# Kernel optimization log

Measured on AMD Instinct MI355X. Metric: run time of the kernel, lower is better.

## Reference

```python
import jax, jax.numpy as jnp
import numpy as np

B, N, M, C = 256, 2048, 64, 512
OUT = 3 * M + 6  # fc_write output: [M,1,1,3,1,M,M]


def setup_inputs() -> dict:
    key = jax.random.key(0)
    k0, k1, k2, k3, k4 = jax.random.split(key, 5)
    xavier = 1.4 * np.sqrt(6.0 / (C + OUT))  # xavier_uniform gain=1.4 scale
    return {
        "h": jax.random.normal(k0, (B, C), jnp.float32),
        "w_prev": jax.nn.softmax(jax.random.normal(k1, (B, N), jnp.float32), axis=1),
        "memory": jax.random.normal(k2, (B, N, M), jnp.float32),
        "W": jax.random.uniform(k3, (OUT, C), jnp.float32, -xavier, xavier),
        "b": 0.01 * jax.random.normal(k4, (OUT,), jnp.float32),
    }


def reference(h, w_prev, memory, W, b):
    # controller projection + split
    o = h @ W.T + b  # [B, 3M+6]
    bounds = np.cumsum([M, 1, 1, 3, 1, M])
    k, beta, g, s, gamma, e, a = jnp.split(o, bounds, axis=1)
    beta = jax.nn.softplus(beta)            # [B,1]
    g = jax.nn.sigmoid(g)                   # [B,1]
    s = jax.nn.softmax(s, axis=1)           # [B,3] shift weights {-1,0,+1}
    gamma = 1.0 + jax.nn.softplus(gamma)    # [B,1]
    e = jax.nn.sigmoid(e)                   # [B,M]

    # content addressing: cosine similarity + softmax
    mem_e = memory + 1e-16
    k_e = k + 1e-16
    sim = jnp.einsum('bnm,bm->bn', mem_e, k_e)
    denom = jnp.maximum(
        jnp.linalg.norm(mem_e, axis=-1) * jnp.linalg.norm(k_e, axis=-1, keepdims=True),
        1e-8,
    )
    w_c = jax.nn.softmax(beta * sim / denom, axis=1)  # [B,N]

    # interpolation gate
    w_g = g * w_c + (1.0 - g) * w_prev

    # circular shift convolution (3 taps)
    w_t = (jnp.roll(w_g, 1, axis=1) * s[:, 0:1]
           + w_g * s[:, 1:2]
           + jnp.roll(w_g, -1, axis=1) * s[:, 2:3])

    # sharpening
    w_s = w_t ** gamma
    w = w_s / (jnp.sum(w_s, axis=1, keepdims=True) + 1e-16)  # [B,N]

    # erase/add memory write
    erase = jnp.einsum('bn,bm->bnm', w, e)
    add = jnp.einsum('bn,bm->bnm', w, a)
    mem_new = memory * (1.0 - erase) + add
    return w, mem_new
```

## Files before the change

### kernel.cpp

```cpp
#include <hip/hip_runtime.h>
#include <stdint.h>

#define BB   256
#define NN   2048
#define MM   64
#define CC   512
#define OUTD 198

typedef float vf4 __attribute__((ext_vector_type(4)));

__device__ __forceinline__ float softplusf(float x) {
    return x > 20.f ? x : log1pf(expf(x));
}
__device__ __forceinline__ float sigmoidf(float x) {
    return 1.f / (1.f + expf(-x));
}

__global__ __launch_bounds__(1024, 4) void k_fused(
        const float* __restrict__ h, const float* __restrict__ Wm,
        const float* __restrict__ bias, const float* __restrict__ w_prev,
        const float* __restrict__ mem, float* __restrict__ w_out,
        float* __restrict__ mem_out) {
    __shared__ float hs[CC];
    __shared__ float os[OUTD];
    __shared__ __align__(16) float kk[MM];
    __shared__ __align__(16) float ee[MM];
    __shared__ __align__(16) float aa[MM];
    __shared__ float sc[8];
    __shared__ float lg[NN];
    __shared__ float wg[NN];
    __shared__ float red[16];

    const int b = blockIdx.x;
    const int t = threadIdx.x;
    const int lane = t & 63;
    const int wid = t >> 6;

    if (t < CC) hs[t] = h[(size_t)b * CC + t];
    __syncthreads();

    if (t < 4 * OUTD) {
        const int row = t >> 2, l4 = t & 3;
        const float* wr = Wm + (size_t)row * CC + 4 * l4;
        float acc = 0.f;
        #pragma unroll
        for (int c = 0; c < CC; c += 16) {
            const float4 p = *(const float4*)(wr + c);
            const int hb = c + 4 * l4;
            acc += p.x * hs[hb] + p.y * hs[hb + 1] + p.z * hs[hb + 2] + p.w * hs[hb + 3];
        }
        acc += __shfl_xor(acc, 1, 64);
        acc += __shfl_xor(acc, 2, 64);
        if (l4 == 0) os[row] = acc + bias[row];
    }
    __syncthreads();

    if (t < 64) {
        const float kv = os[t] + 1e-16f;
        kk[t] = kv;
        float ss = kv * kv;
        #pragma unroll
        for (int off = 32; off; off >>= 1) ss += __shfl_xor(ss, off, 64);
        if (t == 0) sc[3] = sqrtf(ss);
    } else if (t < 128) {
        const int m = t - 64;
        ee[m] = sigmoidf(os[70 + m]);
        aa[m] = os[134 + m];
    } else if (t == 128) {
        sc[0] = softplusf(os[64]);
    } else if (t == 129) {
        sc[1] = sigmoidf(os[65]);
    } else if (t == 130) {
        sc[2] = 1.f + softplusf(os[69]);
    } else if (t == 131) {
        const float x0 = os[66], x1 = os[67], x2 = os[68];
        const float mx = fmaxf(x0, fmaxf(x1, x2));
        const float e0 = expf(x0 - mx), e1 = expf(x1 - mx), e2 = expf(x2 - mx);
        const float inv = 1.f / (e0 + e1 + e2);
        sc[4] = e0 * inv; sc[5] = e1 * inv; sc[6] = e2 * inv;
    }
    __syncthreads();

    {
        const int l = t & 15, grp = t >> 4;
        const float kv0 = kk[4 * l + 0], kv1 = kk[4 * l + 1];
        const float kv2 = kk[4 * l + 2], kv3 = kk[4 * l + 3];
        const float beta = sc[0], knorm = sc[3];
        const float* mb = mem + (size_t)b * NN * MM;
        #pragma unroll 4
        for (int it = 0; it < 32; ++it) {
            const int row = it * 64 + grp;
            const float4 p = *(const float4*)(mb + (size_t)row * MM + 4 * l);
            const float m0 = p.x + 1e-16f, m1 = p.y + 1e-16f;
            const float m2 = p.z + 1e-16f, m3 = p.w + 1e-16f;
            float dot = m0 * kv0 + m1 * kv1 + m2 * kv2 + m3 * kv3;
            float ss  = m0 * m0 + m1 * m1 + m2 * m2 + m3 * m3;
            #pragma unroll
            for (int off = 1; off < 16; off <<= 1) {
                dot += __shfl_xor(dot, off, 64);
                ss  += __shfl_xor(ss,  off, 64);
            }
            if (l == 0)
                lg[row] = beta * dot / fmaxf(sqrtf(ss) * knorm, 1e-8f);
        }
    }
    __syncthreads();

    const float g = sc[1], gamma = sc[2];
    const float s0 = sc[4], s1 = sc[5], s2 = sc[6];

    float v0 = lg[t], v1 = lg[t + 1024];
    float lmax = fmaxf(v0, v1);
    #pragma unroll
    for (int off = 32; off; off >>= 1) lmax = fmaxf(lmax, __shfl_xor(lmax, off, 64));
    if (lane == 0) red[wid] = lmax;
    __syncthreads();
    float mx = red[0];
    #pragma unroll
    for (int i = 1; i < 16; ++i) mx = fmaxf(mx, red[i]);
    __syncthreads();

    v0 = expf(v0 - mx); v1 = expf(v1 - mx);
    float lsum = v0 + v1;
    #pragma unroll
    for (int off = 32; off; off >>= 1) lsum += __shfl_xor(lsum, off, 64);
    if (lane == 0) red[wid] = lsum;
    __syncthreads();
    float tot = 0.f;
    #pragma unroll
    for (int i = 0; i < 16; ++i) tot += red[i];
    __syncthreads();
    const float inv = 1.f / tot;

    wg[t]        = g * (v0 * inv) + (1.f - g) * w_prev[(size_t)b * NN + t];
    wg[t + 1024] = g * (v1 * inv) + (1.f - g) * w_prev[(size_t)b * NN + t + 1024];
    __syncthreads();

    float ws0, ws1;
    {
        const int n0 = t;
        const float wt0 = wg[(n0 + NN - 1) & (NN - 1)] * s0 + wg[n0] * s1
                        + wg[(n0 + 1) & (NN - 1)] * s2;
        ws0 = (wt0 > 0.f) ? exp2f(gamma * log2f(wt0)) : 0.f;
        const int n1 = t + 1024;
        const float wt1 = wg[(n1 - 1) & (NN - 1)] * s0 + wg[n1] * s1
                        + wg[(n1 + 1) & (NN - 1)] * s2;
        ws1 = (wt1 > 0.f) ? exp2f(gamma * log2f(wt1)) : 0.f;
    }
    float psum = ws0 + ws1;
    #pragma unroll
    for (int off = 32; off; off >>= 1) psum += __shfl_xor(psum, off, 64);
    if (lane == 0) red[wid] = psum;
    __syncthreads();
    float ptot = 0.f;
    #pragma unroll
    for (int i = 0; i < 16; ++i) ptot += red[i];
    const float invp = 1.f / (ptot + 1e-16f);

    const float wf0 = ws0 * invp, wf1 = ws1 * invp;
    lg[t] = wf0;
    lg[t + 1024] = wf1;
    w_out[(size_t)b * NN + t] = wf0;
    w_out[(size_t)b * NN + t + 1024] = wf1;
    __syncthreads();

    {
        const int m0 = (4 * t) & 63;
        const vf4 ev = *(const vf4*)(ee + m0);
        const vf4 av = *(const vf4*)(aa + m0);
        const float* mb = mem + (size_t)b * NN * MM + 4 * t;
        float* ob = mem_out + (size_t)b * NN * MM + 4 * t;
        #pragma unroll 8
        for (int it = 0; it < 32; ++it) {
            const float w = lg[it * 64 + (t >> 4)];
            const float4 p = *(const float4*)(mb + it * 4096);
            vf4 o;
            o.x = p.x * (1.f - w * ev.x) + w * av.x;
            o.y = p.y * (1.f - w * ev.y) + w * av.y;
            o.z = p.z * (1.f - w * ev.z) + w * av.z;
            o.w = p.w * (1.f - w * ev.w) + w * av.w;
            __builtin_nontemporal_store(o, (vf4*)(ob + it * 4096));
        }
    }
}

extern "C" void kernel_launch(void* const* d_in, const int* in_sizes, int n_in,
                              void* d_out, int out_size, void* d_ws, size_t ws_size,
                              hipStream_t stream) {
    const float* h      = (const float*)d_in[0];
    const float* w_prev = (const float*)d_in[1];
    const float* memory = (const float*)d_in[2];
    const float* W      = (const float*)d_in[3];
    const float* bias   = (const float*)d_in[4];
    float* out = (float*)d_out;

    float* w_out   = out;
    float* mem_out = out + (size_t)BB * NN;

    k_fused<<<BB, 1024, 0, stream>>>(h, W, bias, w_prev, memory, w_out, mem_out);
}
```

Baseline: 272.1 us.

## Split each batch row across two cooperating blocks with flag-based logit exchange

Launches two blocks per batch row, each computing cosine logits and the memory write for half of the N slots. The halves swap logits through a global workspace using release/acquire flags with magic values, and both blocks then compute the full softmax, shift and sharpen redundantly. This doubles the grid to fill more compute units and halves the streaming work per block. In exchange it adds a memset launch, duplicates the controller projection per block, and relies on partner blocks being co-resident for the spin-wait, which risks deadlock if they are not.

```diff
diff --git a/kernel.cpp b/kernel.cpp
--- a/kernel.cpp
+++ b/kernel.cpp
@@ -7,6 +7,9 @@
 #define CC   512
 #define OUTD 198
 
+#define MAGIC1 0x1B873593u
+#define MAGIC2 0xC2B2AE35u
+
 typedef float vf4 __attribute__((ext_vector_type(4)));
 
 __device__ __forceinline__ float softplusf(float x) {
@@ -16,25 +19,30 @@
     return 1.f / (1.f + expf(-x));
 }
 
-__global__ __launch_bounds__(1024, 4) void k_fused(
+__global__ __launch_bounds__(1024, 8) void k_fused(
         const float* __restrict__ h, const float* __restrict__ Wm,
         const float* __restrict__ bias, const float* __restrict__ w_prev,
         const float* __restrict__ mem, float* __restrict__ w_out,
-        float* __restrict__ mem_out) {
+        float* __restrict__ mem_out, float* __restrict__ ws) {
     __shared__ float hs[CC];
     __shared__ float os[OUTD];
     __shared__ __align__(16) float kk[MM];
     __shared__ __align__(16) float ee[MM];
     __shared__ __align__(16) float aa[MM];
     __shared__ float sc[8];
-    __shared__ float lg[NN];
+    __shared__ float lgs[NN];
     __shared__ float wg[NN];
     __shared__ float red[16];
 
-    const int b = blockIdx.x;
-    const int t = threadIdx.x;
+    const int pb = blockIdx.x;
+    const int b  = pb >> 1;
+    const int hf = pb & 1;
+    const int t  = threadIdx.x;
     const int lane = t & 63;
-    const int wid = t >> 6;
+    const int wid  = t >> 6;
+
+    float* glg = ws;
+    unsigned* flags = (unsigned*)(ws + (size_t)BB * NN);
 
     if (t < CC) hs[t] = h[(size_t)b * CC + t];
     __syncthreads();
@@ -86,11 +94,11 @@
         const float kv0 = kk[4 * l + 0], kv1 = kk[4 * l + 1];
         const float kv2 = kk[4 * l + 2], kv3 = kk[4 * l + 3];
         const float beta = sc[0], knorm = sc[3];
-        const float* mb = mem + (size_t)b * NN * MM;
+        const float* mb = mem + ((size_t)b * NN + hf * 1024) * MM;
         #pragma unroll 4
-        for (int it = 0; it < 32; ++it) {
-            const int row = it * 64 + grp;
-            const float4 p = *(const float4*)(mb + (size_t)row * MM + 4 * l);
+        for (int it = 0; it < 16; ++it) {
+            const int rl = it * 64 + grp;
+            const float4 p = *(const float4*)(mb + (size_t)rl * MM + 4 * l);
             const float m0 = p.x + 1e-16f, m1 = p.y + 1e-16f;
             const float m2 = p.z + 1e-16f, m3 = p.w + 1e-16f;
             float dot = m0 * kv0 + m1 * kv1 + m2 * kv2 + m3 * kv3;
@@ -101,15 +109,33 @@
                 ss  += __shfl_xor(ss,  off, 64);
             }
             if (l == 0)
-                lg[row] = beta * dot / fmaxf(sqrtf(ss) * knorm, 1e-8f);
+                lgs[hf * 1024 + rl] = beta * dot / fmaxf(sqrtf(ss) * knorm, 1e-8f);
         }
+    }
+    __syncthreads();
+
+    glg[(size_t)b * NN + hf * 1024 + t] = lgs[hf * 1024 + t];
+    __threadfence();
+    __syncthreads();
+    if (t == 0) {
+        __hip_atomic_store(&flags[pb],       MAGIC1, __ATOMIC_RELEASE, __HIP_MEMORY_SCOPE_AGENT);
+        __hip_atomic_store(&flags[512 + pb], MAGIC2, __ATOMIC_RELEASE, __HIP_MEMORY_SCOPE_AGENT);
+        while (__hip_atomic_load(&flags[pb ^ 1], __ATOMIC_ACQUIRE, __HIP_MEMORY_SCOPE_AGENT) != MAGIC1 ||
+               __hip_atomic_load(&flags[512 + (pb ^ 1)], __ATOMIC_ACQUIRE, __HIP_MEMORY_SCOPE_AGENT) != MAGIC2)
+            __builtin_amdgcn_s_sleep(2);
+    }
+    __syncthreads();
+    {
+        const int ph = hf ^ 1;
+        const float* src = glg + (size_t)b * NN + ph * 1024;
+        lgs[ph * 1024 + t] = __hip_atomic_load(&src[t], __ATOMIC_RELAXED, __HIP_MEMORY_SCOPE_AGENT);
     }
     __syncthreads();
 
     const float g = sc[1], gamma = sc[2];
     const float s0 = sc[4], s1 = sc[5], s2 = sc[6];
 
-    float v0 = lg[t], v1 = lg[t + 1024];
+    float v0 = lgs[t], v1 = lgs[t + 1024];
     float lmax = fmaxf(v0, v1);
     #pragma unroll
     for (int off = 32; off; off >>= 1) lmax = fmaxf(lmax, __shfl_xor(lmax, off, 64));
@@ -157,29 +183,28 @@
     for (int i = 0; i < 16; ++i) ptot += red[i];
     const float invp = 1.f / (ptot + 1e-16f);
 
-    const float wf0 = ws0 * invp, wf1 = ws1 * invp;
-    lg[t] = wf0;
-    lg[t + 1024] = wf1;
-    w_out[(size_t)b * NN + t] = wf0;
-    w_out[(size_t)b * NN + t + 1024] = wf1;
-    __syncthreads();
-
-    {
-        const int m0 = (4 * t) & 63;
+    const float wf = (hf ? ws1 : ws0) * invp;
+    lgs[t] = wf;
+    w_out[(size_t)b * NN + hf * 1024 + t] = wf;
+    __syncthreads();
+
+    {
+        const int m0 = 4 * (t & 15);
         const vf4 ev = *(const vf4*)(ee + m0);
         const vf4 av = *(const vf4*)(aa + m0);
-        const float* mb = mem + (size_t)b * NN * MM + 4 * t;
-        float* ob = mem_out + (size_t)b * NN * MM + 4 * t;
-        #pragma unroll 8
-        for (int it = 0; it < 32; ++it) {
-            const float w = lg[it * 64 + (t >> 4)];
-            const float4 p = *(const float4*)(mb + it * 4096);
+        const size_t base = ((size_t)b * NN + hf * 1024) * MM + 4 * t;
+        const float* mb = mem + base;
+        float* ob = mem_out + base;
+        #pragma unroll 4
+        for (int it = 0; it < 16; ++it) {
+            const float w = lgs[it * 64 + (t >> 4)];
+            const float4 p = *(const float4*)(mb + (size_t)it * 4096);
             vf4 o;
             o.x = p.x * (1.f - w * ev.x) + w * av.x;
             o.y = p.y * (1.f - w * ev.y) + w * av.y;
             o.z = p.z * (1.f - w * ev.z) + w * av.z;
             o.w = p.w * (1.f - w * ev.w) + w * av.w;
-            __builtin_nontemporal_store(o, (vf4*)(ob + it * 4096));
+            __builtin_nontemporal_store(o, (vf4*)(ob + (size_t)it * 4096));
         }
     }
 }
@@ -193,9 +218,11 @@
     const float* W      = (const float*)d_in[3];
     const float* bias   = (const float*)d_in[4];
     float* out = (float*)d_out;
+    float* ws  = (float*)d_ws;
 
     float* w_out   = out;
     float* mem_out = out + (size_t)BB * NN;
 
-    k_fused<<<BB, 1024, 0, stream>>>(h, W, bias, w_prev, memory, w_out, mem_out);
-}
+    hipMemsetAsync(ws + (size_t)BB * NN, 0, 2 * 512 * sizeof(unsigned), stream);
+    k_fused<<<BB * 2, 1024, 0, stream>>>(h, W, bias, w_prev, memory, w_out, mem_out, ws);
+}
```

Measured after the change: 480.4 us. 1.77x slower.

## Stream memory chunks through LDS with async global_load_lds double buffering

Applied to the files above, without the earlier changes.

Both passes over the memory tensor (cosine-similarity pass and erase/add write pass) now stream 16 KB chunks into a double-buffered LDS stage using global_load_lds DMA, with manual vmcnt waits. The first chunks of the second pass are prefetched while the softmax/shift/sharpen math runs, and w_prev is preloaded into LDS at kernel start. The aim is to hide global load latency and overlap it with reductions. The cost is roughly 32 KB more LDS per block, hand-managed waitcnt ordering that relies on per-wave ownership of LDS slices, and serialised per-chunk waits.

```diff
diff --git a/kernel.cpp b/kernel.cpp
--- a/kernel.cpp
+++ b/kernel.cpp
@@ -7,6 +7,9 @@
 #define CC   512
 #define OUTD 198
 
+#define CHUNK_F 4096
+#define NCH     32
+
 typedef float vf4 __attribute__((ext_vector_type(4)));
 
 __device__ __forceinline__ float softplusf(float x) {
@@ -14,6 +17,19 @@
 }
 __device__ __forceinline__ float sigmoidf(float x) {
     return 1.f / (1.f + expf(-x));
+}
+
+__device__ __forceinline__ void dma16(const float* g, float* l) {
+    __builtin_amdgcn_global_load_lds(
+        (const __attribute__((address_space(1))) uint32_t*)g,
+        (__attribute__((address_space(3))) uint32_t*)l, 16, 0, 0);
+}
+
+__device__ __forceinline__ void bar_lds() {
+    asm volatile("s_waitcnt lgkmcnt(0)" ::: "memory");
+    __builtin_amdgcn_sched_barrier(0);
+    __builtin_amdgcn_s_barrier();
+    __builtin_amdgcn_sched_barrier(0);
 }
 
 __global__ __launch_bounds__(1024, 4) void k_fused(
@@ -21,23 +37,37 @@
         const float* __restrict__ bias, const float* __restrict__ w_prev,
         const float* __restrict__ mem, float* __restrict__ w_out,
         float* __restrict__ mem_out) {
+    __shared__ __align__(16) float stage[2][CHUNK_F];
     __shared__ float hs[CC];
     __shared__ float os[OUTD];
     __shared__ __align__(16) float kk[MM];
     __shared__ __align__(16) float ee[MM];
     __shared__ __align__(16) float aa[MM];
     __shared__ float sc[8];
-    __shared__ float lg[NN];
+    __shared__ float lgs[NN];
     __shared__ float wg[NN];
+    __shared__ float wprev_s[NN];
     __shared__ float red[16];
 
-    const int b = blockIdx.x;
-    const int t = threadIdx.x;
-    const int lane = t & 63;
-    const int wid = t >> 6;
-
-    if (t < CC) hs[t] = h[(size_t)b * CC + t];
-    __syncthreads();
+    const int b  = blockIdx.x;
+    const int t  = threadIdx.x;
+    const int ln = t & 63;
+    const int wv = t >> 6;
+    const int seg  = ln & 15;
+    const int rsub = ln >> 4;
+
+    const float* mb = mem + (size_t)b * (NN * MM);
+
+    float hv = 0.f;
+    if (t < CC) hv = h[(size_t)b * CC + t];
+    const float wp0 = w_prev[(size_t)b * NN + t];
+    const float wp1 = w_prev[(size_t)b * NN + t + 1024];
+    dma16(mb + 0 * CHUNK_F + wv * 256 + ln * 4, &stage[0][wv * 256]);
+    dma16(mb + 1 * CHUNK_F + wv * 256 + ln * 4, &stage[1][wv * 256]);
+    if (t < CC) hs[t] = hv;
+    wprev_s[t] = wp0;
+    wprev_s[t + 1024] = wp1;
+    bar_lds();
 
     if (t < 4 * OUTD) {
         const int row = t >> 2, l4 = t & 3;
@@ -53,7 +83,7 @@
         acc += __shfl_xor(acc, 2, 64);
         if (l4 == 0) os[row] = acc + bias[row];
     }
-    __syncthreads();
+    bar_lds();
 
     if (t < 64) {
         const float kv = os[t] + 1e-16f;
@@ -79,18 +109,17 @@
         const float inv = 1.f / (e0 + e1 + e2);
         sc[4] = e0 * inv; sc[5] = e1 * inv; sc[6] = e2 * inv;
     }
-    __syncthreads();
+    bar_lds();
 
     {
-        const int l = t & 15, grp = t >> 4;
-        const float kv0 = kk[4 * l + 0], kv1 = kk[4 * l + 1];
-        const float kv2 = kk[4 * l + 2], kv3 = kk[4 * l + 3];
+        const float kv0 = kk[4 * seg + 0], kv1 = kk[4 * seg + 1];
+        const float kv2 = kk[4 * seg + 2], kv3 = kk[4 * seg + 3];
         const float beta = sc[0], knorm = sc[3];
-        const float* mb = mem + (size_t)b * NN * MM;
-        #pragma unroll 4
-        for (int it = 0; it < 32; ++it) {
-            const int row = it * 64 + grp;
-            const float4 p = *(const float4*)(mb + (size_t)row * MM + 4 * l);
+        for (int c = 0; c < NCH; ++c) {
+            if (c < NCH - 1) { asm volatile("s_waitcnt vmcnt(1)" ::: "memory"); }
+            else             { asm volatile("s_waitcnt vmcnt(0)" ::: "memory"); }
+            __builtin_amdgcn_sched_barrier(0);
+            const float4 p = *(const float4*)&stage[c & 1][wv * 256 + ln * 4];
             const float m0 = p.x + 1e-16f, m1 = p.y + 1e-16f;
             const float m2 = p.z + 1e-16f, m3 = p.w + 1e-16f;
             float dot = m0 * kv0 + m1 * kv1 + m2 * kv2 + m3 * kv3;
@@ -100,41 +129,47 @@
                 dot += __shfl_xor(dot, off, 64);
                 ss  += __shfl_xor(ss,  off, 64);
             }
-            if (l == 0)
-                lg[row] = beta * dot / fmaxf(sqrtf(ss) * knorm, 1e-8f);
+            if (seg == 0)
+                lgs[c * 64 + wv * 4 + rsub] =
+                    beta * dot / fmaxf(sqrtf(ss) * knorm, 1e-8f);
+            if (c + 2 < NCH)
+                dma16(mb + (size_t)(c + 2) * CHUNK_F + wv * 256 + ln * 4,
+                      &stage[c & 1][wv * 256]);
         }
     }
-    __syncthreads();
+    dma16(mb + 0 * CHUNK_F + wv * 256 + ln * 4, &stage[0][wv * 256]);
+    dma16(mb + 1 * CHUNK_F + wv * 256 + ln * 4, &stage[1][wv * 256]);
+    bar_lds();
 
     const float g = sc[1], gamma = sc[2];
     const float s0 = sc[4], s1 = sc[5], s2 = sc[6];
 
-    float v0 = lg[t], v1 = lg[t + 1024];
+    float v0 = lgs[t], v1 = lgs[t + 1024];
     float lmax = fmaxf(v0, v1);
     #pragma unroll
     for (int off = 32; off; off >>= 1) lmax = fmaxf(lmax, __shfl_xor(lmax, off, 64));
-    if (lane == 0) red[wid] = lmax;
-    __syncthreads();
+    if (ln == 0) red[wv] = lmax;
+    bar_lds();
     float mx = red[0];
     #pragma unroll
     for (int i = 1; i < 16; ++i) mx = fmaxf(mx, red[i]);
-    __syncthreads();
+    bar_lds();
 
     v0 = expf(v0 - mx); v1 = expf(v1 - mx);
     float lsum = v0 + v1;
     #pragma unroll
     for (int off = 32; off; off >>= 1) lsum += __shfl_xor(lsum, off, 64);
-    if (lane == 0) red[wid] = lsum;
-    __syncthreads();
+    if (ln == 0) red[wv] = lsum;
+    bar_lds();
     float tot = 0.f;
     #pragma unroll
     for (int i = 0; i < 16; ++i) tot += red[i];
-    __syncthreads();
+    bar_lds();
     const float inv = 1.f / tot;
 
-    wg[t]        = g * (v0 * inv) + (1.f - g) * w_prev[(size_t)b * NN + t];
-    wg[t + 1024] = g * (v1 * inv) + (1.f - g) * w_prev[(size_t)b * NN + t + 1024];
-    __syncthreads();
+    wg[t]        = g * (v0 * inv) + (1.f - g) * wprev_s[t];
+    wg[t + 1024] = g * (v1 * inv) + (1.f - g) * wprev_s[t + 1024];
+    bar_lds();
 
     float ws0, ws1;
     {
@@ -150,36 +185,40 @@
     float psum = ws0 + ws1;
     #pragma unroll
     for (int off = 32; off; off >>= 1) psum += __shfl_xor(psum, off, 64);
-    if (lane == 0) red[wid] = psum;
-    __syncthreads();
+    if (ln == 0) red[wv] = psum;
+    bar_lds();
     float ptot = 0.f;
     #pragma unroll
     for (int i = 0; i < 16; ++i) ptot += red[i];
     const float invp = 1.f / (ptot + 1e-16f);
 
     const float wf0 = ws0 * invp, wf1 = ws1 * invp;
-    lg[t] = wf0;
-    lg[t + 1024] = wf1;
+    lgs[t] = wf0;
+    lgs[t + 1024] = wf1;
     w_out[(size_t)b * NN + t] = wf0;
     w_out[(size_t)b * NN + t + 1024] = wf1;
-    __syncthreads();
+    bar_lds();
 
     {
-        const int m0 = (4 * t) & 63;
-        const vf4 ev = *(const vf4*)(ee + m0);
-        const vf4 av = *(const vf4*)(aa + m0);
-        const float* mb = mem + (size_t)b * NN * MM + 4 * t;
-        float* ob = mem_out + (size_t)b * NN * MM + 4 * t;
-        #pragma unroll 8
-        for (int it = 0; it < 32; ++it) {
-            const float w = lg[it * 64 + (t >> 4)];
-            const float4 p = *(const float4*)(mb + it * 4096);
+        const vf4 ev = *(const vf4*)&ee[4 * seg];
+        const vf4 av = *(const vf4*)&aa[4 * seg];
+        float* ob = mem_out + (size_t)b * (NN * MM);
+        for (int c = 0; c < NCH; ++c) {
+            if (c < NCH - 1) { asm volatile("s_waitcnt vmcnt(2)" ::: "memory"); }
+            else             { asm volatile("s_waitcnt vmcnt(0)" ::: "memory"); }
+            __builtin_amdgcn_sched_barrier(0);
+            const float wq = lgs[c * 64 + wv * 4 + rsub];
+            const float4 p = *(const float4*)&stage[c & 1][wv * 256 + ln * 4];
             vf4 o;
-            o.x = p.x * (1.f - w * ev.x) + w * av.x;
-            o.y = p.y * (1.f - w * ev.y) + w * av.y;
-            o.z = p.z * (1.f - w * ev.z) + w * av.z;
-            o.w = p.w * (1.f - w * ev.w) + w * av.w;
-            __builtin_nontemporal_store(o, (vf4*)(ob + it * 4096));
+            o.x = p.x * (1.f - wq * ev.x) + wq * av.x;
+            o.y = p.y * (1.f - wq * ev.y) + wq * av.y;
+            o.z = p.z * (1.f - wq * ev.z) + wq * av.z;
+            o.w = p.w * (1.f - wq * ev.w) + wq * av.w;
+            __builtin_nontemporal_store(
+                o, (vf4*)(ob + (size_t)c * CHUNK_F + wv * 256 + ln * 4));
+            if (c + 2 < NCH)
+                dma16(mb + (size_t)(c + 2) * CHUNK_F + wv * 256 + ln * 4,
+                      &stage[c & 1][wv * 256]);
         }
     }
 }
```

Measured after the change: 269.0 us. About the same (-1.1%).

## Split fused per-batch kernel into four grid-wide kernels with chunked softmax partials

Applied to the files above, without the earlier changes.

Replaces the single 256-block kernel (one 1024-thread block per batch row) with four kernels that each launch 2048 blocks of 256 threads, every block handling a 256-row chunk of one batch. Softmax and sharpening normalisation are combined through per-chunk max/sum partials kept in workspace memory. The aim is to fill the GPU with more, smaller blocks instead of 256 large serial ones. In exchange it adds three extra kernel launches, workspace round-trips, and a second full read of memory in the write pass that may no longer hit cache.

```diff
diff --git a/kernel.cpp b/kernel.cpp
--- a/kernel.cpp
+++ b/kernel.cpp
@@ -7,6 +7,13 @@
 #define CC   512
 #define OUTD 198
 
+#define OS_STRIDE 200
+#define OS_OFF    0
+#define LG_OFF    (BB * OS_STRIDE)
+#define MXP_OFF   (LG_OFF + BB * NN)
+#define SEP_OFF   (MXP_OFF + BB * 8)
+#define PTP_OFF   (SEP_OFF + BB * 8)
+
 typedef float vf4 __attribute__((ext_vector_type(4)));
 
 __device__ __forceinline__ float softplusf(float x) {
@@ -16,171 +23,194 @@
     return 1.f / (1.f + expf(-x));
 }
 
-__global__ __launch_bounds__(1024, 4) void k_fused(
+__device__ __forceinline__ float bred_max(float v, float* red) {
+    #pragma unroll
+    for (int off = 32; off; off >>= 1) v = fmaxf(v, __shfl_down(v, off, 64));
+    if ((threadIdx.x & 63) == 0) red[threadIdx.x >> 6] = v;
+    __syncthreads();
+    float r = fmaxf(fmaxf(red[0], red[1]), fmaxf(red[2], red[3]));
+    __syncthreads();
+    return r;
+}
+__device__ __forceinline__ float bred_sum(float v, float* red) {
+    #pragma unroll
+    for (int off = 32; off; off >>= 1) v += __shfl_down(v, off, 64);
+    if ((threadIdx.x & 63) == 0) red[threadIdx.x >> 6] = v;
+    __syncthreads();
+    float r = red[0] + red[1] + red[2] + red[3];
+    __syncthreads();
+    return r;
+}
+
+__global__ __launch_bounds__(256, 8) void k_ctrl(
         const float* __restrict__ h, const float* __restrict__ Wm,
-        const float* __restrict__ bias, const float* __restrict__ w_prev,
-        const float* __restrict__ mem, float* __restrict__ w_out,
-        float* __restrict__ mem_out) {
+        const float* __restrict__ bias, float* __restrict__ ws) {
     __shared__ float hs[CC];
-    __shared__ float os[OUTD];
-    __shared__ __align__(16) float kk[MM];
-    __shared__ __align__(16) float ee[MM];
-    __shared__ __align__(16) float aa[MM];
-    __shared__ float sc[8];
-    __shared__ float lg[NN];
-    __shared__ float wg[NN];
-    __shared__ float red[16];
-
-    const int b = blockIdx.x;
-    const int t = threadIdx.x;
-    const int lane = t & 63;
-    const int wid = t >> 6;
-
-    if (t < CC) hs[t] = h[(size_t)b * CC + t];
-    __syncthreads();
-
-    if (t < 4 * OUTD) {
-        const int row = t >> 2, l4 = t & 3;
-        const float* wr = Wm + (size_t)row * CC + 4 * l4;
+    const int b = blockIdx.x >> 3, c = blockIdx.x & 7, t = threadIdx.x;
+    hs[t]       = h[(size_t)b * CC + t];
+    hs[t + 256] = h[(size_t)b * CC + t + 256];
+    __syncthreads();
+
+    const int slot = t >> 3, l8 = t & 7;
+    const int r = c * 25 + slot;
+    if (slot < 25 && r < OUTD) {
+        const float* wr = Wm + (size_t)r * CC + l8 * 64;
+        const float* hp = hs + l8 * 64;
         float acc = 0.f;
         #pragma unroll
-        for (int c = 0; c < CC; c += 16) {
-            const float4 p = *(const float4*)(wr + c);
-            const int hb = c + 4 * l4;
-            acc += p.x * hs[hb] + p.y * hs[hb + 1] + p.z * hs[hb + 2] + p.w * hs[hb + 3];
+        for (int q = 0; q < 16; ++q) {
+            const float4 p = *(const float4*)(wr + q * 4);
+            acc += p.x * hp[q*4+0] + p.y * hp[q*4+1] + p.z * hp[q*4+2] + p.w * hp[q*4+3];
         }
         acc += __shfl_xor(acc, 1, 64);
         acc += __shfl_xor(acc, 2, 64);
-        if (l4 == 0) os[row] = acc + bias[row];
-    }
-    __syncthreads();
+        acc += __shfl_xor(acc, 4, 64);
+        if (l8 == 0) ws[OS_OFF + b * OS_STRIDE + r] = acc + bias[r];
+    }
+}
+
+__global__ __launch_bounds__(256, 8) void k_logits(
+        const float* __restrict__ mem, float* __restrict__ ws) {
+    __shared__ __align__(16) float kk[MM];
+    __shared__ float sc[2];
+    __shared__ float lgl[256];
+    __shared__ float red[4];
+    const int b = blockIdx.x >> 3, c = blockIdx.x & 7, t = threadIdx.x;
+    const float* osb = ws + OS_OFF + (size_t)b * OS_STRIDE;
 
     if (t < 64) {
-        const float kv = os[t] + 1e-16f;
+        const float kv = osb[t] + 1e-16f;
         kk[t] = kv;
         float ss = kv * kv;
         #pragma unroll
         for (int off = 32; off; off >>= 1) ss += __shfl_xor(ss, off, 64);
-        if (t == 0) sc[3] = sqrtf(ss);
-    } else if (t < 128) {
-        const int m = t - 64;
-        ee[m] = sigmoidf(os[70 + m]);
-        aa[m] = os[134 + m];
-    } else if (t == 128) {
-        sc[0] = softplusf(os[64]);
-    } else if (t == 129) {
-        sc[1] = sigmoidf(os[65]);
-    } else if (t == 130) {
-        sc[2] = 1.f + softplusf(os[69]);
-    } else if (t == 131) {
-        const float x0 = os[66], x1 = os[67], x2 = os[68];
-        const float mx = fmaxf(x0, fmaxf(x1, x2));
-        const float e0 = expf(x0 - mx), e1 = expf(x1 - mx), e2 = expf(x2 - mx);
-        const float inv = 1.f / (e0 + e1 + e2);
-        sc[4] = e0 * inv; sc[5] = e1 * inv; sc[6] = e2 * inv;
-    }
-    __syncthreads();
-
-    {
-        const int l = t & 15, grp = t >> 4;
-        const float kv0 = kk[4 * l + 0], kv1 = kk[4 * l + 1];
-        const float kv2 = kk[4 * l + 2], kv3 = kk[4 * l + 3];
-        const float beta = sc[0], knorm = sc[3];
-        const float* mb = mem + (size_t)b * NN * MM;
-        #pragma unroll 4
-        for (int it = 0; it < 32; ++it) {
-            const int row = it * 64 + grp;
-            const float4 p = *(const float4*)(mb + (size_t)row * MM + 4 * l);
-            const float m0 = p.x + 1e-16f, m1 = p.y + 1e-16f;
-            const float m2 = p.z + 1e-16f, m3 = p.w + 1e-16f;
-            float dot = m0 * kv0 + m1 * kv1 + m2 * kv2 + m3 * kv3;
-            float ss  = m0 * m0 + m1 * m1 + m2 * m2 + m3 * m3;
-            #pragma unroll
-            for (int off = 1; off < 16; off <<= 1) {
-                dot += __shfl_xor(dot, off, 64);
-                ss  += __shfl_xor(ss,  off, 64);
-            }
-            if (l == 0)
-                lg[row] = beta * dot / fmaxf(sqrtf(ss) * knorm, 1e-8f);
+        if (t == 0) sc[0] = sqrtf(ss);
+    } else if (t == 64) {
+        sc[1] = softplusf(osb[64]);
+    }
+    __syncthreads();
+
+    const int l = t & 15, grp = t >> 4;
+    float kv0 = kk[4*l+0], kv1 = kk[4*l+1], kv2 = kk[4*l+2], kv3 = kk[4*l+3];
+    const float beta = sc[1], knorm = sc[0];
+    const int row0 = c * 256;
+    #pragma unroll
+    for (int it = 0; it < 16; ++it) {
+        const int row = row0 + it * 16 + grp;
+        const float4 p = *(const float4*)(mem + ((size_t)b * NN + row) * MM + 4 * l);
+        const float m0 = p.x + 1e-16f, m1 = p.y + 1e-16f;
+        const float m2 = p.z + 1e-16f, m3 = p.w + 1e-16f;
+        float dot = m0 * kv0 + m1 * kv1 + m2 * kv2 + m3 * kv3;
+        float ss  = m0 * m0 + m1 * m1 + m2 * m2 + m3 * m3;
+        #pragma unroll
+        for (int off = 1; off < 16; off <<= 1) {
+            dot += __shfl_xor(dot, off, 64);
+            ss  += __shfl_xor(ss,  off, 64);
         }
-    }
-    __syncthreads();
-
-    const float g = sc[1], gamma = sc[2];
-    const float s0 = sc[4], s1 = sc[5], s2 = sc[6];
-
-    float v0 = lg[t], v1 = lg[t + 1024];
-    float lmax = fmaxf(v0, v1);
-    #pragma unroll
-    for (int off = 32; off; off >>= 1) lmax = fmaxf(lmax, __shfl_xor(lmax, off, 64));
-    if (lane == 0) red[wid] = lmax;
-    __syncthreads();
-    float mx = red[0];
-    #pragma unroll
-    for (int i = 1; i < 16; ++i) mx = fmaxf(mx, red[i]);
-    __syncthreads();
-
-    v0 = expf(v0 - mx); v1 = expf(v1 - mx);
-    float lsum = v0 + v1;
-    #pragma unroll
-    for (int off = 32; off; off >>= 1) lsum += __shfl_xor(lsum, off, 64);
-    if (lane == 0) red[wid] = lsum;
-    __syncthreads();
-    float tot = 0.f;
-    #pragma unroll
-    for (int i = 0; i < 16; ++i) tot += red[i];
-    __syncthreads();
-    const float inv = 1.f / tot;
-
-    wg[t]        = g * (v0 * inv) + (1.f - g) * w_prev[(size_t)b * NN + t];
-    wg[t + 1024] = g * (v1 * inv) + (1.f - g) * w_prev[(size_t)b * NN + t + 1024];
-    __syncthreads();
-
-    float ws0, ws1;
-    {
-        const int n0 = t;
-        const float wt0 = wg[(n0 + NN - 1) & (NN - 1)] * s0 + wg[n0] * s1
-                        + wg[(n0 + 1) & (NN - 1)] * s2;
-        ws0 = (wt0 > 0.f) ? exp2f(gamma * log2f(wt0)) : 0.f;
-        const int n1 = t + 1024;
-        const float wt1 = wg[(n1 - 1) & (NN - 1)] * s0 + wg[n1] * s1
-                        + wg[(n1 + 1) & (NN - 1)] * s2;
-        ws1 = (wt1 > 0.f) ? exp2f(gamma * log2f(wt1)) : 0.f;
-    }
-    float psum = ws0 + ws1;
-    #pragma unroll
-    for (int off = 32; off; off >>= 1) psum += __shfl_xor(psum, off, 64);
-    if (lane == 0) red[wid] = psum;
-    __syncthreads();
-    float ptot = 0.f;
-    #pragma unroll
-    for (int i = 0; i < 16; ++i) ptot += red[i];
-    const float invp = 1.f / (ptot + 1e-16f);
-
-    const float wf0 = ws0 * invp, wf1 = ws1 * invp;
-    lg[t] = wf0;
-    lg[t + 1024] = wf1;
-    w_out[(size_t)b * NN + t] = wf0;
-    w_out[(size_t)b * NN + t + 1024] = wf1;
-    __syncthreads();
-
-    {
-        const int m0 = (4 * t) & 63;
-        const vf4 ev = *(const vf4*)(ee + m0);
-        const vf4 av = *(const vf4*)(aa + m0);
-        const float* mb = mem + (size_t)b * NN * MM + 4 * t;
-        float* ob = mem_out + (size_t)b * NN * MM + 4 * t;
-        #pragma unroll 8
-        for (int it = 0; it < 32; ++it) {
-            const float w = lg[it * 64 + (t >> 4)];
-            const float4 p = *(const float4*)(mb + it * 4096);
-            vf4 o;
-            o.x = p.x * (1.f - w * ev.x) + w * av.x;
-            o.y = p.y * (1.f - w * ev.y) + w * av.y;
-            o.z = p.z * (1.f - w * ev.z) + w * av.z;
-            o.w = p.w * (1.f - w * ev.w) + w * av.w;
-            __builtin_nontemporal_store(o, (vf4*)(ob + it * 4096));
+        if (l == 0) {
+            const float lgv = beta * dot / fmaxf(sqrtf(ss) * knorm, 1e-8f);
+            ws[LG_OFF + (size_t)b * NN + row] = lgv;
+            lgl[it * 16 + grp] = lgv;
         }
+    }
+    __syncthreads();
+
+    const float v  = lgl[t];
+    const float mx = bred_max(v, red);
+    const float se = bred_sum(expf(v - mx), red);
+    if (t == 0) {
+        ws[MXP_OFF + b * 8 + c] = mx;
+        ws[SEP_OFF + b * 8 + c] = se;
+    }
+}
+
+__global__ __launch_bounds__(256, 8) void k_sharp(
+        const float* __restrict__ w_prev, float* __restrict__ ws,
+        float* __restrict__ w_out) {
+    __shared__ float wgc[258];
+    __shared__ float sc[7];
+    __shared__ float red[4];
+    const int b = blockIdx.x >> 3, c = blockIdx.x & 7, t = threadIdx.x;
+    const float* osb = ws + OS_OFF + (size_t)b * OS_STRIDE;
+
+    if (t == 0) {
+        sc[0] = sigmoidf(osb[65]);
+        sc[1] = 1.f + softplusf(osb[69]);
+        const float x0 = osb[66], x1 = osb[67], x2 = osb[68];
+        const float m3 = fmaxf(x0, fmaxf(x1, x2));
+        const float e0 = expf(x0 - m3), e1 = expf(x1 - m3), e2 = expf(x2 - m3);
+        const float i3 = 1.f / (e0 + e1 + e2);
+        sc[2] = e0 * i3; sc[3] = e1 * i3; sc[4] = e2 * i3;
+        float mx = -1e30f;
+        #pragma unroll
+        for (int j = 0; j < 8; ++j) mx = fmaxf(mx, ws[MXP_OFF + b * 8 + j]);
+        float tot = 0.f;
+        #pragma unroll
+        for (int j = 0; j < 8; ++j)
+            tot += ws[SEP_OFF + b * 8 + j] * expf(ws[MXP_OFF + b * 8 + j] - mx);
+        sc[5] = mx; sc[6] = 1.f / tot;
+    }
+    __syncthreads();
+    const float g = sc[0], gamma = sc[1];
+    const float s0 = sc[2], s1 = sc[3], s2 = sc[4];
+    const float mx = sc[5], invtot = sc[6];
+
+    for (int j = t; j < 258; j += 256) {
+        const int r = (c * 256 - 1 + j) & (NN - 1);
+        const float wc = expf(ws[LG_OFF + (size_t)b * NN + r] - mx) * invtot;
+        wgc[j] = g * wc + (1.f - g) * w_prev[(size_t)b * NN + r];
+    }
+    __syncthreads();
+
+    const float wt = wgc[t] * s0 + wgc[t + 1] * s1 + wgc[t + 2] * s2;
+    const float wsv = (wt > 0.f) ? exp2f(gamma * log2f(wt)) : 0.f;
+    w_out[(size_t)b * NN + c * 256 + t] = wsv;
+    const float ps = bred_sum(wsv, red);
+    if (t == 0) ws[PTP_OFF + b * 8 + c] = ps;
+}
+
+__global__ __launch_bounds__(256, 8) void k_write(
+        const float* __restrict__ mem, const float* __restrict__ ws,
+        float* __restrict__ w_out, float* __restrict__ mem_out) {
+    __shared__ float wrow[256];
+    __shared__ __align__(16) float ee[MM], aa[MM];
+    __shared__ float scp[1];
+    const int b = blockIdx.x >> 3, c = blockIdx.x & 7, t = threadIdx.x;
+    const float* osb = ws + OS_OFF + (size_t)b * OS_STRIDE;
+
+    if (t == 0) {
+        float pt = 0.f;
+        #pragma unroll
+        for (int j = 0; j < 8; ++j) pt += ws[PTP_OFF + b * 8 + j];
+        scp[0] = 1.f / (pt + 1e-16f);
+    } else if (t >= 64 && t < 128) {
+        ee[t - 64] = sigmoidf(osb[70 + (t - 64)]);
+    } else if (t >= 128 && t < 192) {
+        aa[t - 128] = osb[134 + (t - 128)];
+    }
+    __syncthreads();
+
+    const float wv = w_out[(size_t)b * NN + c * 256 + t] * scp[0];
+    wrow[t] = wv;
+    w_out[(size_t)b * NN + c * 256 + t] = wv;
+    __syncthreads();
+
+    const int seg = t & 15, rs = t >> 4;
+    const vf4 ev = *(const vf4*)&ee[4 * seg];
+    const vf4 av = *(const vf4*)&aa[4 * seg];
+    const float* mb = mem + ((size_t)b * NN + c * 256) * MM + 4 * seg;
+    float* ob = mem_out + ((size_t)b * NN + c * 256) * MM + 4 * seg;
+    #pragma unroll 4
+    for (int it = 0; it < 16; ++it) {
+        const int rr = it * 16 + rs;
+        const float w = wrow[rr];
+        const float4 p = *(const float4*)(mb + (size_t)rr * MM);
+        vf4 o;
+        o.x = p.x * (1.f - w * ev.x) + w * av.x;
+        o.y = p.y * (1.f - w * ev.y) + w * av.y;
+        o.z = p.z * (1.f - w * ev.z) + w * av.z;
+        o.w = p.w * (1.f - w * ev.w) + w * av.w;
+        __builtin_nontemporal_store(o, (vf4*)(ob + (size_t)rr * MM));
     }
 }
 
@@ -193,9 +223,13 @@
     const float* W      = (const float*)d_in[3];
     const float* bias   = (const float*)d_in[4];
     float* out = (float*)d_out;
+    float* ws  = (float*)d_ws;
 
     float* w_out   = out;
     float* mem_out = out + (size_t)BB * NN;
 
-    k_fused<<<BB, 1024, 0, stream>>>(h, W, bias, w_prev, memory, w_out, mem_out);
-}
+    k_ctrl  <<<BB * 8, 256, 0, stream>>>(h, W, bias, ws);
+    k_logits<<<BB * 8, 256, 0, stream>>>(memory, ws);
+    k_sharp <<<BB * 8, 256, 0, stream>>>(w_prev, ws, w_out);
+    k_write <<<BB * 8, 256, 0, stream>>>(memory, ws, w_out, mem_out);
+}
```

After: 285.4 us. 1.05x slower.
